# Performance work log

Hardware: AMD Instinct MI355X
Metric: run time of the kernel (lower is better)

## Reference

```python
import jax, jax.numpy as jnp
import numpy as np

B, S, E, HD = 32, 1024, 768, 64


def _rope_tables(seq_len, dim):
    # theta = 10000 ** (-2*arange(0,dim,2)/dim); freqs = pos * theta
    theta = jnp.power(10000.0, -2.0 * jnp.arange(0, dim, 2, dtype=jnp.float32) / dim)
    pos = jnp.arange(seq_len, dtype=jnp.float32)[:, None]          # [S,1]
    freqs = pos * theta[None, :]                                    # [S,dim//2]
    cos = jnp.repeat(jnp.cos(freqs), 2, axis=-1)                    # [S,dim]
    sin = jnp.repeat(jnp.sin(freqs), 2, axis=-1)                    # [S,dim]
    return cos, sin


def _apply_rope(x, cos, sin):
    # rotate-half interleaved: new[...,0::2] = -x[...,1::2]; new[...,1::2] = x[...,0::2]
    b, s, d = x.shape
    x2 = x.reshape(b, s, d // 2, 2)
    rot = jnp.stack([-x2[..., 1], x2[..., 0]], axis=-1).reshape(b, s, d)
    return x * cos[None] + rot * sin[None]


def setup_inputs() -> dict:
    key = jax.random.key(0)
    k0, k1, k2, k3 = jax.random.split(key, 4)
    x = jax.random.normal(k0, (B, S, E), dtype=jnp.float32)
    Wq = jax.random.normal(k1, (HD, E), dtype=jnp.float32) * 0.02
    Wk = jax.random.normal(k2, (HD, E), dtype=jnp.float32) * 0.02
    Wv = jax.random.normal(k3, (HD, E), dtype=jnp.float32) * 0.02
    return {"x": x, "Wq": Wq, "Wk": Wk, "Wv": Wv}


def reference(x, Wq, Wk, Wv):
    b, s, e = x.shape
    q = jnp.einsum('bse,he->bsh', x, Wq)
    k = jnp.einsum('bse,he->bsh', x, Wk)
    v = jnp.einsum('bse,he->bsh', x, Wv)
    cos, sin = _rope_tables(s, q.shape[-1])
    rq = _apply_rope(q, cos, sin)
    rk = _apply_rope(k, cos, sin)
    scale = e ** (-0.5)  # NOTE: original scales by emb_dim, not head_size
    scores = jnp.einsum('bqh,bkh->bqk', rq, rk) * scale
    causal = jnp.tril(jnp.ones((s, s), dtype=bool))
    scores = jnp.where(causal[None], scores, -jnp.inf)
    attn = jax.nn.softmax(scores, axis=-1)
    return jnp.einsum('bqk,bkh->bqh', attn, v)
```

## Files before the change

### kernel.cpp

```cpp
#include <hip/hip_runtime.h>
#include <hip/hip_bf16.h>

#define B_  32
#define S_  1024
#define E_  768
#define HD_ 64
#define M_  (B_*S_)

typedef __attribute__((ext_vector_type(8))) short short8;
typedef __attribute__((ext_vector_type(4))) float float4v;

__device__ __forceinline__ unsigned short f2bf(float x) {
    union { float f; unsigned u; } c; c.f = x;
    unsigned r = (c.u + 0x7FFFu + ((c.u >> 16) & 1u)) >> 16;
    return (unsigned short)r;
}

__device__ __forceinline__ void gld_lds16(const void* g, void* l) {
    __builtin_amdgcn_global_load_lds(
        (const __attribute__((address_space(1))) unsigned int*)g,
        (__attribute__((address_space(3))) unsigned int*)l,
        16, 0, 0);
}

__global__ __launch_bounds__(256) void setup_kernel(
    const unsigned int* __restrict__ xw,
    const void* __restrict__ Wq_, const void* __restrict__ Wk_,
    const void* __restrict__ Wv_,
    unsigned int* __restrict__ flag,
    float* __restrict__ cs_t, float* __restrict__ sn_t,
    unsigned short* __restrict__ wp)
{
    const int bx = blockIdx.x;
    if (bx < 128) {
        int idx = bx * 256 + threadIdx.x;
        int pos = idx >> 5;
        int ii  = idx & 31;
        float theta = exp2f(-(float)ii * 0.8304820237218406f);
        float fr = (float)pos * theta;
        float sn, cs;
        sincosf(fr, &sn, &cs);
        cs_t[idx] = cs;
        sn_t[idx] = sn;
        return;
    }
    __shared__ int cnt;
    if (threadIdx.x == 0) cnt = 0;
    __syncthreads();
    unsigned int w0 = xw[(size_t)threadIdx.x * 33331];
    unsigned int e0 = (w0 >> 8) & 0x7F;
    int hit = (e0 >= 0x3B && e0 <= 0x40) ? 1 : 0;
    atomicAdd(&cnt, hit);
    __syncthreads();
    const bool isb = (cnt > 128);
    if (bx == 128) {
        if (threadIdx.x == 0) *flag = isb ? 1u : 0u;
        return;
    }
    int gid  = (bx - 129) * 256 + threadIdx.x;
    int lane = gid & 63;
    int tIdx = gid >> 6;
    int ct   = tIdx / 24;
    int rem  = tIdx - ct * 24;
    int c    = rem >> 1, ks = rem & 1;
    int quad = lane >> 4, l15 = lane & 15;
    const void* wsel = (ct < 4) ? Wq_ : (ct < 8 ? Wk_ : Wv_);
    int row = (ct & 3) * 16 + l15;
    int col = c * 64 + ks * 32 + quad * 8;
    uint4 w;
    if (isb) {
        w = *(const uint4*)((const unsigned short*)wsel + (size_t)row * E_ + col);
    } else {
        const float* f = (const float*)wsel + (size_t)row * E_ + col;
        float4 a = *(const float4*)f, bq = *(const float4*)(f + 4);
        w.x = f2bf(a.x)  | ((unsigned)f2bf(a.y)  << 16);
        w.y = f2bf(a.z)  | ((unsigned)f2bf(a.w)  << 16);
        w.z = f2bf(bq.x) | ((unsigned)f2bf(bq.y) << 16);
        w.w = f2bf(bq.z) | ((unsigned)f2bf(bq.w) << 16);
    }
    *(uint4*)(wp + (size_t)gid * 8) = w;
}

__global__ __launch_bounds__(512, 4) void qkv_mfma_kernel(
    const void* __restrict__ x_, const unsigned short* __restrict__ wp,
    const unsigned int* __restrict__ flag,
    const float* __restrict__ cs_t, const float* __restrict__ sn_t,
    unsigned short* __restrict__ rq_p, unsigned short* __restrict__ rk_p,
    unsigned short* __restrict__ vt_p)
{
    __shared__ __align__(16) char alds[3][8192];

    const bool isb = (*flag != 0);
    const int t    = threadIdx.x;
    const int lane = t & 63;
    const int wave = t >> 6;
    const int quad = lane >> 4;
    const int l15  = lane & 15;
    const int row0 = blockIdx.x * 64;
    const int h    = wave >> 2;
    const int cw   = wave & 3;

    const unsigned aRow = (unsigned)(wave * 8 + (lane >> 3));
    const unsigned eoA  = aRow * 768u + (unsigned)(((lane & 7) ^ (lane >> 3)) * 8);

    unsigned aA[2][2];
    #pragma unroll
    for (int mtl = 0; mtl < 2; ++mtl) {
        unsigned rl = (unsigned)((h * 2 + mtl) * 16 + l15);
        #pragma unroll
        for (int ks = 0; ks < 2; ++ks)
            aA[mtl][ks] = rl * 128u + ((((unsigned)ks << 2) | (unsigned)quad) ^ (rl & 7u)) * 16u;
    }

    const unsigned short* wbase[3][2];
    #pragma unroll
    for (int nt = 0; nt < 3; ++nt) {
        int ct = cw * 3 + nt;
        #pragma unroll
        for (int ks = 0; ks < 2; ++ks)
            wbase[nt][ks] = wp + ((size_t)(ct * 24 + ks)) * 512 + lane * 8;
    }

    float4v acc[3][2];
    #pragma unroll
    for (int nt = 0; nt < 3; ++nt)
        #pragma unroll
        for (int mtl = 0; mtl < 2; ++mtl)
            #pragma unroll
            for (int r = 0; r < 4; ++r) acc[nt][mtl][r] = 0.f;

    short8 breg[2][3][2];

    const unsigned short* xb16 = (const unsigned short*)x_ + (size_t)row0 * E_;
    const float*          xb32 = (const float*)x_ + (size_t)row0 * E_;

    #define LOADB(cc, sel)                                                       \
        {   int tc_ = (cc) < 11 ? (cc) : 11;                                     \
            _Pragma("unroll")                                                    \
            for (int nt_ = 0; nt_ < 3; ++nt_)                                    \
                _Pragma("unroll")                                                \
                for (int ks_ = 0; ks_ < 2; ++ks_)                                \
                    breg[sel][nt_][ks_] =                                        \
                        *(const short8*)(wbase[nt_][ks_] + tc_ * 1024);          \
        }

    #define COMPUTE(cc, sel)                                                     \
        {   const char* sb_ = alds[(cc) % 3];                                    \
            _Pragma("unroll")                                                    \
            for (int ks_ = 0; ks_ < 2; ++ks_) {                                  \
                short8 af0 = *(const short8*)(sb_ + aA[0][ks_]);                 \
                short8 af1 = *(const short8*)(sb_ + aA[1][ks_]);                 \
                _Pragma("unroll")                                                \
                for (int nt_ = 0; nt_ < 3; ++nt_) {                              \
                    acc[nt_][0] = __builtin_amdgcn_mfma_f32_16x16x32_bf16(       \
                        af0, breg[sel][nt_][ks_], acc[nt_][0], 0, 0, 0);         \
                    acc[nt_][1] = __builtin_amdgcn_mfma_f32_16x16x32_bf16(       \
                        af1, breg[sel][nt_][ks_], acc[nt_][1], 0, 0, 0);         \
                }                                                                \
            }                                                                    \
        }

    if (isb) {
        LOADB(0, 0);
        __builtin_amdgcn_sched_barrier(0);
        gld_lds16(xb16 + eoA,      alds[0] + wave * 1024);
        gld_lds16(xb16 + eoA + 64, alds[1] + wave * 1024);
        __builtin_amdgcn_sched_barrier(0);
        #pragma unroll
        for (int c = 0; c < 12; ++c) {
            asm volatile("s_waitcnt vmcnt(1)" ::: "memory");
            __builtin_amdgcn_s_barrier();
            LOADB(c + 1, (c + 1) & 1);
            __builtin_amdgcn_sched_barrier(0);
            {
                int tc = (c + 2) < 11 ? (c + 2) : 11;
                gld_lds16(xb16 + eoA + tc * 64, alds[(c + 2) % 3] + wave * 1024);
            }
            __builtin_amdgcn_sched_barrier(0);
            COMPUTE(c, c & 1);
        }
    } else {
        auto stageA_f = [&](int c) {
            const float* f = xb32 + eoA + c * 64;
            float4 a = *(const float4*)f, bq = *(const float4*)(f + 4);
            uint4 w;
            w.x = f2bf(a.x)  | ((unsigned)f2bf(a.y)  << 16);
            w.y = f2bf(a.z)  | ((unsigned)f2bf(a.w)  << 16);
            w.z = f2bf(bq.x) | ((unsigned)f2bf(bq.y) << 16);
            w.w = f2bf(bq.z) | ((unsigned)f2bf(bq.w) << 16);
            *(uint4*)(alds[c % 3] + wave * 1024 + (size_t)lane * 16) = w;
        };
        stageA_f(0); stageA_f(1);
        LOADB(0, 0);
        __syncthreads();
        #pragma unroll
        for (int c = 0; c < 12; ++c) {
            if (c + 2 < 12) stageA_f(c + 2);
            LOADB(c + 1, (c + 1) & 1);
            COMPUTE(c, c & 1);
            __syncthreads();
        }
    }
    #undef LOADB
    #undef COMPUTE

    const int b      = row0 >> 10;
    const int s_in_b = row0 & (S_ - 1);
    #pragma unroll
    for (int nt = 0; nt < 3; ++nt) {
        int ct = cw * 3 + nt;
        int region = ct >> 2;
        int d = (ct & 3) * 16 + l15;
        if (region < 2) {
            unsigned short* dst = (region == 0) ? rq_p : rk_p;
            int ii = d >> 1;
            int ksq = d >> 5, quadq = (d >> 3) & 3, e = d & 7;
            #pragma unroll
            for (int mtl = 0; mtl < 2; ++mtl) {
                #pragma unroll
                for (int r = 0; r < 4; ++r) {
                    int row = row0 + (h * 2 + mtl) * 16 + quad * 4 + r;
                    int pos = row & (S_ - 1);
                    float cs = cs_t[pos * 32 + ii];
                    float sn = sn_t[pos * 32 + ii];
                    float val = acc[nt][mtl][r];
                    float partner = __shfl_xor(val, 1);
                    float res = (d & 1) ? fmaf(val, cs,  partner * sn)
                                        : fmaf(val, cs, -partner * sn);
                    int kt = pos >> 6, ntq = (pos >> 4) & 3, l15q = pos & 15;
                    size_t idx = ((((size_t)(b * 16 + kt) * 4 + ntq) * 2 + ksq) * 64
                                  + quadq * 16 + l15q) * 8 + e;
                    dst[idx] = f2bf(res);
                }
            }
        } else {
            int ntv = ct & 3;
            #pragma unroll
            for (int mtl = 0; mtl < 2; ++mtl) {
                int sb2 = s_in_b + (h * 2 + mtl) * 16 + quad * 4;
                int kt = sb2 >> 6, ksv = (sb2 >> 5) & 1, quadv = (sb2 >> 3) & 3, e0 = sb2 & 7;
                ushort4 pk;
                pk.x = f2bf(acc[nt][mtl][0]);
                pk.y = f2bf(acc[nt][mtl][1]);
                pk.z = f2bf(acc[nt][mtl][2]);
                pk.w = f2bf(acc[nt][mtl][3]);
                size_t idx = ((((size_t)(b * 16 + kt) * 4 + ntv) * 2 + ksv) * 64
                              + quadv * 16 + l15) * 8 + e0;
                *(ushort4*)(vt_p + idx) = pk;
            }
        }
    }
}

__global__ __launch_bounds__(256, 2) void attn_mfma_kernel(
    const unsigned short* __restrict__ rq_p, const unsigned short* __restrict__ rk_p,
    const unsigned short* __restrict__ vt_p, const unsigned int* __restrict__ flag,
    void* __restrict__ out)
{
    __shared__ __align__(16) unsigned short kv[2][32 * 512];
    __shared__ unsigned short plds[4][16][72];

    const bool isb = (*flag != 0);
    const int t    = threadIdx.x;
    const int lane = t & 63;
    const int wave = t >> 6;
    const int quad = lane >> 4;
    const int l15  = lane & 15;
    const int qt   = blockIdx.x;
    const int b    = blockIdx.y;
    const int q0   = qt * 64 + wave * 16;
    const float scale = 0.03608439182435161f;

    const unsigned short* qb = rq_p + ((size_t)((b * 16 + qt) * 4 + wave) * 2) * 512;
    short8 qf0 = *(const short8*)(qb + lane * 8);
    short8 qf1 = *(const short8*)(qb + 512 + lane * 8);

    const unsigned short* sbase[8];
    unsigned eo[8];
    int      slotv[8], tidv[8];
    #pragma unroll
    for (int i = 0; i < 8; ++i) {
        int tid = wave * 8 + i;
        tidv[i] = tid;
        int isV  = tid >> 4;
        int rem  = tid & 15;
        int slot = rem >> 3;
        int wi   = rem & 7;
        int nt   = wi >> 1, ks = wi & 1;
        slotv[i] = slot;
        sbase[i] = isV ? vt_p : rk_p;
        eo[i]    = (unsigned)(((b * 64 + nt) * 2 + ks) * 512 + lane * 8);
    }

    float4v o[4];
    float m_[4], l_[4];
    #pragma unroll
    for (int nt = 0; nt < 4; ++nt)
        #pragma unroll
        for (int r = 0; r < 4; ++r) o[nt][r] = 0.f;
    #pragma unroll
    for (int r = 0; r < 4; ++r) { m_[r] = -1e30f; l_[r] = 0.f; }

    const int nIter = (qt + 2) >> 1;

    auto stage = [&](int it, int bsel) {
        int ta  = 2 * it;
        int tb  = min(ta + 1, qt);
        #pragma unroll
        for (int i = 0; i < 8; ++i) {
            int kt = slotv[i] ? tb : ta;
            gld_lds16(sbase[i] + eo[i] + (size_t)kt * 4096,
                      &kv[bsel][(size_t)tidv[i] * 512]);
        }
    };

    stage(0, 0);
    int buf = 0;
    for (int i = 0; i < nIter; ++i) {
        __syncthreads();
        if (i + 1 < nIter) stage(i + 1, buf ^ 1);
        const unsigned short* kb = kv[buf];

        float sc[2][4][4];
        #pragma unroll
        for (int slot = 0; slot < 2; ++slot) {
            #pragma unroll
            for (int nt = 0; nt < 4; ++nt) {
                float4v s;
                #pragma unroll
                for (int r = 0; r < 4; ++r) s[r] = 0.f;
                short8 kf0 = *(const short8*)(kb + (size_t)(slot * 8 + nt * 2 + 0) * 512 + lane * 8);
                short8 kf1 = *(const short8*)(kb + (size_t)(slot * 8 + nt * 2 + 1) * 512 + lane * 8);
                s = __builtin_amdgcn_mfma_f32_16x16x32_bf16(qf0, kf0, s, 0, 0, 0);
                s = __builtin_amdgcn_mfma_f32_16x16x32_bf16(qf1, kf1, s, 0, 0, 0);
                #pragma unroll
                for (int r = 0; r < 4; ++r) sc[slot][nt][r] = s[r] * scale;
            }
        }

        if (2 * i + 1 >= qt) {
            #pragma unroll
            for (int slot = 0; slot < 2; ++slot) {
                int ktl = 2 * i + slot;
                #pragma unroll
                for (int nt = 0; nt < 4; ++nt) {
                    int kg = ktl * 64 + nt * 16 + l15;
                    #pragma unroll
                    for (int r = 0; r < 4; ++r) {
                        int qg = q0 + quad * 4 + r;
                        if (kg > qg) sc[slot][nt][r] = -1e30f;
                    }
                }
            }
        }

        float mx[4];
        #pragma unroll
        for (int r = 0; r < 4; ++r) {
            float a0 = fmaxf(fmaxf(sc[0][0][r], sc[0][1][r]), fmaxf(sc[0][2][r], sc[0][3][r]));
            float a1 = fmaxf(fmaxf(sc[1][0][r], sc[1][1][r]), fmaxf(sc[1][2][r], sc[1][3][r]));
            mx[r] = fmaxf(a0, a1);
        }
        #pragma unroll
        for (int st = 1; st < 16; st <<= 1)
            #pragma unroll
            for (int r = 0; r < 4; ++r)
                mx[r] = fmaxf(mx[r], __shfl_xor(mx[r], st));

        float al[4];
        #pragma unroll
        for (int r = 0; r < 4; ++r) {
            float mn = fmaxf(m_[r], mx[r]);
            al[r] = __expf(m_[r] - mn);
            m_[r] = mn;
        }

        float sm[4] = {0.f, 0.f, 0.f, 0.f};
        #pragma unroll
        for (int slot = 0; slot < 2; ++slot)
            #pragma unroll
            for (int nt = 0; nt < 4; ++nt)
                #pragma unroll
                for (int r = 0; r < 4; ++r) {
                    float p = __expf(sc[slot][nt][r] - m_[r]);
                    sc[slot][nt][r] = p;
                    sm[r] += p;
                }
        #pragma unroll
        for (int st = 1; st < 16; st <<= 1)
            #pragma unroll
            for (int r = 0; r < 4; ++r)
                sm[r] += __shfl_xor(sm[r], st);
        #pragma unroll
        for (int r = 0; r < 4; ++r) l_[r] = l_[r] * al[r] + sm[r];

        #pragma unroll
        for (int nt = 0; nt < 4; ++nt)
            #pragma unroll
            for (int r = 0; r < 4; ++r) o[nt][r] *= al[r];

        #pragma unroll
        for (int slot = 0; slot < 2; ++slot) {
            #pragma unroll
            for (int nt = 0; nt < 4; ++nt)
                #pragma unroll
                for (int r = 0; r < 4; ++r)
                    plds[wave][quad * 4 + r][nt * 16 + l15] = f2bf(sc[slot][nt][r]);
            short8 pf0 = *(const short8*)&plds[wave][l15][quad * 8];
            short8 pf1 = *(const short8*)&plds[wave][l15][32 + quad * 8];
            #pragma unroll
            for (int nt = 0; nt < 4; ++nt) {
                short8 vf0 = *(const short8*)(kb + (size_t)(16 + slot * 8 + nt * 2 + 0) * 512 + lane * 8);
                short8 vf1 = *(const short8*)(kb + (size_t)(16 + slot * 8 + nt * 2 + 1) * 512 + lane * 8);
                o[nt] = __builtin_amdgcn_mfma_f32_16x16x32_bf16(pf0, vf0, o[nt], 0, 0, 0);
                o[nt] = __builtin_amdgcn_mfma_f32_16x16x32_bf16(pf1, vf1, o[nt], 0, 0, 0);
            }
        }
        buf ^= 1;
    }

    float inv[4];
    #pragma unroll
    for (int r = 0; r < 4; ++r) inv[r] = 1.0f / l_[r];
    if (isb) {
        unsigned short* op = (unsigned short*)out;
        #pragma unroll
        for (int nt = 0; nt < 4; ++nt)
            #pragma unroll
            for (int r = 0; r < 4; ++r) {
                size_t row = (size_t)b * S_ + q0 + quad * 4 + r;
                op[row * HD_ + nt * 16 + l15] = f2bf(o[nt][r] * inv[r]);
            }
    } else {
        float* op = (float*)out;
        #pragma unroll
        for (int nt = 0; nt < 4; ++nt)
            #pragma unroll
            for (int r = 0; r < 4; ++r) {
                size_t row = (size_t)b * S_ + q0 + quad * 4 + r;
                op[row * HD_ + nt * 16 + l15] = o[nt][r] * inv[r];
            }
    }
}

extern "C" void kernel_launch(void* const* d_in, const int* in_sizes, int n_in,
                              void* d_out, int out_size, void* d_ws, size_t ws_size,
                              hipStream_t stream) {
    const void* x  = d_in[0];
    const void* Wq = d_in[1];
    const void* Wk = d_in[2];
    const void* Wv = d_in[3];

    unsigned int* flag = (unsigned int*)d_ws;
    float* cs_t = (float*)d_ws + 64;
    float* sn_t = cs_t + (size_t)S_ * 32;
    unsigned short* wp   = (unsigned short*)(sn_t + (size_t)S_ * 32);
    unsigned short* rq_p = wp + (size_t)288 * 512;
    unsigned short* rk_p = rq_p + (size_t)M_ * HD_;
    unsigned short* vt_p = rk_p + (size_t)M_ * HD_;

    hipLaunchKernelGGL(setup_kernel, dim3(201), dim3(256), 0, stream,
                       (const unsigned int*)x, Wq, Wk, Wv, flag, cs_t, sn_t, wp);
    hipLaunchKernelGGL(qkv_mfma_kernel, dim3(M_ / 64), dim3(512), 0, stream,
                       x, wp, flag, cs_t, sn_t, rq_p, rk_p, vt_p);
    hipLaunchKernelGGL(attn_mfma_kernel, dim3(S_ / 64, B_), dim3(256), 0, stream,
                       rq_p, rk_p, vt_p, flag, d_out);
}
```

Measured before the change: 194.8 us.

## Load K/V fragments directly from global into registers, drop LDS double buffer

Removes the shared-memory double-buffered K/V staging via global_load_lds and the per-iteration block barrier. Each wave now loads its K and V MFMA fragments straight from global memory into registers, with the V loads issued before the softmax so their latency can overlap. This cuts LDS capacity use, which may allow more resident blocks, and removes the synchronisation. The cost is that all four waves redundantly fetch the same K/V tiles from global or L2, and register pressure rises from the 32 short8 fragments held per iteration.

```diff
diff --git a/kernel.cpp b/kernel.cpp
--- a/kernel.cpp
+++ b/kernel.cpp
@@ -257,7 +257,6 @@
     const unsigned short* __restrict__ vt_p, const unsigned int* __restrict__ flag,
     void* __restrict__ out)
 {
-    __shared__ __align__(16) unsigned short kv[2][32 * 512];
     __shared__ unsigned short plds[4][16][72];
 
     const bool isb = (*flag != 0);
@@ -275,22 +274,8 @@
     short8 qf0 = *(const short8*)(qb + lane * 8);
     short8 qf1 = *(const short8*)(qb + 512 + lane * 8);
 
-    const unsigned short* sbase[8];
-    unsigned eo[8];
-    int      slotv[8], tidv[8];
-    #pragma unroll
-    for (int i = 0; i < 8; ++i) {
-        int tid = wave * 8 + i;
-        tidv[i] = tid;
-        int isV  = tid >> 4;
-        int rem  = tid & 15;
-        int slot = rem >> 3;
-        int wi   = rem & 7;
-        int nt   = wi >> 1, ks = wi & 1;
-        slotv[i] = slot;
-        sbase[i] = isV ? vt_p : rk_p;
-        eo[i]    = (unsigned)(((b * 64 + nt) * 2 + ks) * 512 + lane * 8);
-    }
+    const unsigned short* kb0 = rk_p + ((size_t)b * 128) * 512 + lane * 8;
+    const unsigned short* vb0 = vt_p + ((size_t)b * 128) * 512 + lane * 8;
 
     float4v o[4];
     float m_[4], l_[4];
@@ -303,23 +288,20 @@
 
     const int nIter = (qt + 2) >> 1;
 
-    auto stage = [&](int it, int bsel) {
-        int ta  = 2 * it;
-        int tb  = min(ta + 1, qt);
-        #pragma unroll
-        for (int i = 0; i < 8; ++i) {
-            int kt = slotv[i] ? tb : ta;
-            gld_lds16(sbase[i] + eo[i] + (size_t)kt * 4096,
-                      &kv[bsel][(size_t)tidv[i] * 512]);
-        }
-    };
-
-    stage(0, 0);
-    int buf = 0;
     for (int i = 0; i < nIter; ++i) {
-        __syncthreads();
-        if (i + 1 < nIter) stage(i + 1, buf ^ 1);
-        const unsigned short* kb = kv[buf];
+        const int ta = 2 * i;
+        const int tb = min(ta + 1, qt);
+        const int ktv[2] = { ta, tb };
+
+        short8 kf[2][4][2];
+        #pragma unroll
+        for (int slot = 0; slot < 2; ++slot)
+            #pragma unroll
+            for (int nt = 0; nt < 4; ++nt)
+                #pragma unroll
+                for (int ks = 0; ks < 2; ++ks)
+                    kf[slot][nt][ks] = *(const short8*)(
+                        kb0 + (size_t)(ktv[slot] * 8 + nt * 2 + ks) * 512);
 
         float sc[2][4][4];
         #pragma unroll
@@ -329,14 +311,22 @@
                 float4v s;
                 #pragma unroll
                 for (int r = 0; r < 4; ++r) s[r] = 0.f;
-                short8 kf0 = *(const short8*)(kb + (size_t)(slot * 8 + nt * 2 + 0) * 512 + lane * 8);
-                short8 kf1 = *(const short8*)(kb + (size_t)(slot * 8 + nt * 2 + 1) * 512 + lane * 8);
-                s = __builtin_amdgcn_mfma_f32_16x16x32_bf16(qf0, kf0, s, 0, 0, 0);
-                s = __builtin_amdgcn_mfma_f32_16x16x32_bf16(qf1, kf1, s, 0, 0, 0);
+                s = __builtin_amdgcn_mfma_f32_16x16x32_bf16(qf0, kf[slot][nt][0], s, 0, 0, 0);
+                s = __builtin_amdgcn_mfma_f32_16x16x32_bf16(qf1, kf[slot][nt][1], s, 0, 0, 0);
                 #pragma unroll
                 for (int r = 0; r < 4; ++r) sc[slot][nt][r] = s[r] * scale;
             }
         }
+
+        short8 vf[2][4][2];
+        #pragma unroll
+        for (int slot = 0; slot < 2; ++slot)
+            #pragma unroll
+            for (int nt = 0; nt < 4; ++nt)
+                #pragma unroll
+                for (int ks = 0; ks < 2; ++ks)
+                    vf[slot][nt][ks] = *(const short8*)(
+                        vb0 + (size_t)(ktv[slot] * 8 + nt * 2 + ks) * 512);
 
         if (2 * i + 1 >= qt) {
             #pragma unroll
@@ -410,13 +400,10 @@
             short8 pf1 = *(const short8*)&plds[wave][l15][32 + quad * 8];
             #pragma unroll
             for (int nt = 0; nt < 4; ++nt) {
-                short8 vf0 = *(const short8*)(kb + (size_t)(16 + slot * 8 + nt * 2 + 0) * 512 + lane * 8);
-                short8 vf1 = *(const short8*)(kb + (size_t)(16 + slot * 8 + nt * 2 + 1) * 512 + lane * 8);
-                o[nt] = __builtin_amdgcn_mfma_f32_16x16x32_bf16(pf0, vf0, o[nt], 0, 0, 0);
-                o[nt] = __builtin_amdgcn_mfma_f32_16x16x32_bf16(pf1, vf1, o[nt], 0, 0, 0);
-            }
-        }
-        buf ^= 1;
+                o[nt] = __builtin_amdgcn_mfma_f32_16x16x32_bf16(pf0, vf[slot][nt][0], o[nt], 0, 0, 0);
+                o[nt] = __builtin_amdgcn_mfma_f32_16x16x32_bf16(pf1, vf[slot][nt][1], o[nt], 0, 0, 0);
+            }
+        }
     }
 
     float inv[4];
```

New measurement: 190.6 us. 1.02x faster.
